# Kernel optimization log

Hardware: AMD Instinct MI355X
Metric: run time of the kernel (lower is better)

The kernel has to match this reference:

```python
import jax, jax.numpy as jnp
import numpy as np

B, XD, PD, D, H = 512, 32768, 512, 64, 128  # batch, x_dim, proj_dim, latent_dim, per_dim_hidden
G1 = 1024  # gene projector hidden (hardcoded in module)


def _init(k, shape, fan_in):
    s = 1.0 / np.sqrt(fan_in)
    return jax.random.uniform(k, shape, jnp.float32, -s, s)


def setup_inputs() -> dict:
    key = jax.random.key(0)
    ks = jax.random.split(key, 16)
    return {
        "x": jax.random.normal(ks[0], (B, XD), jnp.float32),
        "z": jax.random.normal(ks[1], (B, D), jnp.float32),
        "perm": jax.random.permutation(ks[2], B).astype(jnp.int32),
        # shared gene projector
        "Wg1": _init(ks[3], (XD, G1), XD), "bg1": _init(ks[4], (G1,), XD),
        "Wg2": _init(ks[5], (G1, PD), G1), "bg2": _init(ks[6], (PD,), G1),
        # per-dimension 3-layer MLPs, stacked over D. Layer-1 weight [PD+1, H]
        # is split into the h-part Wh and the z-part Wz (last input column).
        "Wh": _init(ks[7], (D, PD, H), PD + 1),
        "Wz": _init(ks[8], (D, H), PD + 1),
        "b1": _init(ks[9], (D, H), PD + 1),
        "W2": _init(ks[10], (D, H, H), H), "b2": _init(ks[11], (D, H), H),
        "W3": _init(ks[12], (D, H), H), "b3": _init(ks[13], (D,), H),
    }


def reference(x, z, perm, Wg1, bg1, Wg2, bg2, Wh, Wz, b1, W2, b2, W3, b3):
    elu = jax.nn.elu
    # shared gene projector (eval mode: dropout = identity, no noise)
    h = elu(elu(x @ Wg1 + bg1) @ Wg2 + bg2)            # [B, PD]
    # batched layer-1 of all D per-dim nets; h-projection computed once and
    # reused for the marginal pass via permutation (h_shuffled = h[perm]).
    hWh = jnp.einsum('bp,dph->bdh', h, Wh)             # [B, D, H]
    zWz = z[:, :, None] * Wz[None]                     # [B, D, H]

    def head(a1_pre):
        a1 = elu(a1_pre)                               # [B, D, H]
        a2 = elu(jnp.einsum('bdh,dhk->bdk', a1, W2) + b2)
        return jnp.einsum('bdh,dh->bd', a2, W3) + b3   # [B, D] scalar scores

    joint_score = head(hWh + zWz + b1)                 # T(h, z_j)
    marg_score = head(hWh[perm] + zWz + b1)            # T(h_shuffled, z_j)

    emas = jnp.ones((D,), x.dtype)                     # buffer init = ones, eval: no update
    et = jnp.mean(jnp.exp(marg_score), axis=0)         # [D]
    mi = jnp.mean(joint_score, axis=0) - jnp.log(et / emas)
    return -jnp.mean(mi)
```

## Files before the change

### kernel.cpp

```cpp
#include <hip/hip_runtime.h>
#include <hip/hip_bf16.h>
#include <math.h>

#define B_  512
#define XD_ 32768
#define PD_ 512
#define D_  64
#define H_  128
#define G1_ 1024

typedef __attribute__((ext_vector_type(8))) short short8v;
typedef __attribute__((ext_vector_type(4))) float floatx4;

__device__ __forceinline__ float eluf(float v) { return v > 0.f ? v : expm1f(v); }

__device__ __forceinline__ void split8t(const float* c, short8v& h, short8v& l) {
    unsigned hu[8], lu[8];
    #pragma unroll
    for (int j = 0; j < 8; j++) {
        unsigned u = __float_as_uint(c[j]);
        hu[j] = u & 0xFFFF0000u;
        float res = c[j] - __uint_as_float(hu[j]);
        lu[j] = __float_as_uint(res);
    }
    uint4 hp, lp;
    hp.x = __builtin_amdgcn_perm(hu[1], hu[0], 0x07060302u);
    hp.y = __builtin_amdgcn_perm(hu[3], hu[2], 0x07060302u);
    hp.z = __builtin_amdgcn_perm(hu[5], hu[4], 0x07060302u);
    hp.w = __builtin_amdgcn_perm(hu[7], hu[6], 0x07060302u);
    lp.x = __builtin_amdgcn_perm(lu[1], lu[0], 0x07060302u);
    lp.y = __builtin_amdgcn_perm(lu[3], lu[2], 0x07060302u);
    lp.z = __builtin_amdgcn_perm(lu[5], lu[4], 0x07060302u);
    lp.w = __builtin_amdgcn_perm(lu[7], lu[6], 0x07060302u);
    h = __builtin_bit_cast(short8v, hp);
    l = __builtin_bit_cast(short8v, lp);
}

__global__ __launch_bounds__(256, 2) void k_gemm1m(const float* __restrict__ x,
                                                   const float* __restrict__ Wg1,
                                                   float* __restrict__ part,
                                                   int KS) {
    __shared__ ushort Ah[4 * 128 * 8], Al[4 * 128 * 8];
    __shared__ ushort Bh[4 * 128 * 8], Bl[4 * 128 * 8];
    const int nt = blockIdx.x, mt = blockIdx.y, ks = blockIdx.z;
    const int t = threadIdx.x;
    const int w = t >> 6, lane = t & 63;
    const int q = lane >> 4, l15 = lane & 15;
    const int wr = w >> 1, wc = w & 1;
    const int kbB = t >> 6, nb = t & 63;
    const int mA = t & 127, kbA = t >> 7;
    const int k0 = ks * KS;

    const float* Ag = x + (size_t)(mt * 128 + mA) * XD_ + k0 + kbA * 8;
    const float* Bg = Wg1 + (size_t)(k0 + kbB * 8) * G1_ + nt * 128 + nb * 2;

    floatx4 acc[4][4];
    #pragma unroll
    for (int i = 0; i < 4; i++)
        #pragma unroll
        for (int j = 0; j < 4; j++) acc[i][j] = (floatx4){0.f, 0.f, 0.f, 0.f};

    float4 pa0 = *(const float4*)(Ag);
    float4 pa1 = *(const float4*)(Ag + 4);
    float4 pa2 = *(const float4*)(Ag + 16);
    float4 pa3 = *(const float4*)(Ag + 20);
    float2 pb[8];
    #pragma unroll
    for (int kk = 0; kk < 8; kk++) pb[kk] = *(const float2*)(Bg + (size_t)kk * G1_);

    for (int kt = 0; kt < KS; kt += 32) {
        float cA0[8] = {pa0.x, pa0.y, pa0.z, pa0.w, pa1.x, pa1.y, pa1.z, pa1.w};
        float cA1[8] = {pa2.x, pa2.y, pa2.z, pa2.w, pa3.x, pa3.y, pa3.z, pa3.w};
        float c0[8], c1[8];
        #pragma unroll
        for (int kk = 0; kk < 8; kk++) { c0[kk] = pb[kk].x; c1[kk] = pb[kk].y; }
        short8v ah0, al0, ah1, al1, bh0, bl0, bh1, bl1;
        split8t(cA0, ah0, al0);
        split8t(cA1, ah1, al1);
        split8t(c0, bh0, bl0);
        split8t(c1, bh1, bl1);
        if (kt + 32 < KS) {
            pa0 = *(const float4*)(Ag + kt + 32);
            pa1 = *(const float4*)(Ag + kt + 36);
            pa2 = *(const float4*)(Ag + kt + 48);
            pa3 = *(const float4*)(Ag + kt + 52);
            const float* p = Bg + (size_t)(kt + 32) * G1_;
            #pragma unroll
            for (int kk = 0; kk < 8; kk++) pb[kk] = *(const float2*)(p + (size_t)kk * G1_);
        }
        {
            int ia0 = (kbA * 128 + (mA ^ kbA)) * 8;
            int ia1 = ((kbA + 2) * 128 + (mA ^ (kbA + 2))) * 8;
            *(short8v*)&Ah[ia0] = ah0; *(short8v*)&Al[ia0] = al0;
            *(short8v*)&Ah[ia1] = ah1; *(short8v*)&Al[ia1] = al1;
            int n0i = nb * 2;
            int i0 = (kbB * 128 + (n0i ^ kbB)) * 8;
            int i1 = (kbB * 128 + ((n0i + 1) ^ kbB)) * 8;
            *(short8v*)&Bh[i0] = bh0; *(short8v*)&Bl[i0] = bl0;
            *(short8v*)&Bh[i1] = bh1; *(short8v*)&Bl[i1] = bl1;
        }
        __syncthreads();
        short8v af[4], alf[4], bf[4], blf[4];
        #pragma unroll
        for (int i = 0; i < 4; i++) {
            int m = wr * 64 + i * 16 + l15;
            int idx = (q * 128 + (m ^ q)) * 8;
            af[i]  = *(const short8v*)&Ah[idx];
            alf[i] = *(const short8v*)&Al[idx];
        }
        #pragma unroll
        for (int j = 0; j < 4; j++) {
            int n = wc * 64 + j * 16 + l15;
            int idx = (q * 128 + (n ^ q)) * 8;
            bf[j]  = *(const short8v*)&Bh[idx];
            blf[j] = *(const short8v*)&Bl[idx];
        }
        #pragma unroll
        for (int i = 0; i < 4; i++)
            #pragma unroll
            for (int j = 0; j < 4; j++) {
                acc[i][j] = __builtin_amdgcn_mfma_f32_16x16x32_bf16(af[i],  bf[j],  acc[i][j], 0, 0, 0);
                acc[i][j] = __builtin_amdgcn_mfma_f32_16x16x32_bf16(af[i],  blf[j], acc[i][j], 0, 0, 0);
                acc[i][j] = __builtin_amdgcn_mfma_f32_16x16x32_bf16(alf[i], bf[j],  acc[i][j], 0, 0, 0);
            }
        __syncthreads();
    }
    float* P = part + (size_t)ks * (B_ * G1_) + (size_t)(mt * 128) * G1_ + nt * 128;
    #pragma unroll
    for (int i = 0; i < 4; i++)
        #pragma unroll
        for (int j = 0; j < 4; j++) {
            int col = wc * 64 + j * 16 + l15;
            #pragma unroll
            for (int r = 0; r < 4; r++) {
                int row = wr * 64 + i * 16 + q * 4 + r;
                P[(size_t)row * G1_ + col] = acc[i][j][r];
            }
        }
}

__global__ __launch_bounds__(256) void k_red1(const float* __restrict__ part,
                                              const float* __restrict__ bg1,
                                              ushort* __restrict__ Gh,
                                              ushort* __restrict__ Gl,
                                              int nparts) {
    int idx = (blockIdx.x * 256 + threadIdx.x) * 8;
    const int S = B_ * G1_;
    float c[8] = {};
    for (int k = 0; k < nparts; k++) {
        const float* p = part + (size_t)k * S + idx;
        float4 v0 = *(const float4*)p, v1 = *(const float4*)(p + 4);
        c[0] += v0.x; c[1] += v0.y; c[2] += v0.z; c[3] += v0.w;
        c[4] += v1.x; c[5] += v1.y; c[6] += v1.z; c[7] += v1.w;
    }
    int cb = idx & (G1_ - 1);
    float4 b0 = *(const float4*)(bg1 + cb), b1v = *(const float4*)(bg1 + cb + 4);
    c[0] = eluf(c[0] + b0.x); c[1] = eluf(c[1] + b0.y);
    c[2] = eluf(c[2] + b0.z); c[3] = eluf(c[3] + b0.w);
    c[4] = eluf(c[4] + b1v.x); c[5] = eluf(c[5] + b1v.y);
    c[6] = eluf(c[6] + b1v.z); c[7] = eluf(c[7] + b1v.w);
    short8v h, l; split8t(c, h, l);
    *(short8v*)(Gh + idx) = h;
    *(short8v*)(Gl + idx) = l;
}

__global__ __launch_bounds__(256, 2) void k_gemm2m(const ushort* __restrict__ Gh,
                                                   const ushort* __restrict__ Gl,
                                                   const float* __restrict__ Wg2,
                                                   float* __restrict__ part2) {
    __shared__ ushort Ah[4 * 64 * 8], Al[4 * 64 * 8];
    __shared__ ushort Bh[4 * 64 * 8], Bl[4 * 64 * 8];
    const int nt = blockIdx.x, mt = blockIdx.y, ks = blockIdx.z;
    const int t = threadIdx.x;
    const int w = t >> 6, lane = t & 63;
    const int q = lane >> 4, l15 = lane & 15;
    const int kb = (t >> 4) & 3;
    const int rb = (t & 15) | (w << 4);
    const int k0 = ks * 128;

    const int cB = t & 63, g = t >> 6;

    floatx4 acc[4];
    #pragma unroll
    for (int i = 0; i < 4; i++) acc[i] = (floatx4){0.f, 0.f, 0.f, 0.f};

    for (int kt = 0; kt < 128; kt += 32) {
        {
            const ushort* pH = Gh + (size_t)(mt * 64 + rb) * G1_ + k0 + kt + kb * 8;
            const ushort* pL = Gl + (size_t)(mt * 64 + rb) * G1_ + k0 + kt + kb * 8;
            uint4 vh = *(const uint4*)pH;
            uint4 vl = *(const uint4*)pL;
            int idx = (kb * 64 + (rb ^ kb)) * 8;
            *(uint4*)&Ah[idx] = vh;
            *(uint4*)&Al[idx] = vl;
        }
        {
            float c[8];
            const float* p = Wg2 + (size_t)(k0 + kt + g * 8) * PD_ + nt * 64 + cB;
            #pragma unroll
            for (int kk = 0; kk < 8; kk++) c[kk] = p[(size_t)kk * PD_];
            short8v h, l; split8t(c, h, l);
            int idx = (g * 64 + (cB ^ g)) * 8;
            *(short8v*)&Bh[idx] = h;
            *(short8v*)&Bl[idx] = l;
        }
        __syncthreads();
        short8v af[4], alf[4], bf, blf;
        #pragma unroll
        for (int i = 0; i < 4; i++) {
            int m = i * 16 + l15;
            int idx = (q * 64 + (m ^ q)) * 8;
            af[i]  = *(const short8v*)&Ah[idx];
            alf[i] = *(const short8v*)&Al[idx];
        }
        {
            int n = w * 16 + l15;
            int idx = (q * 64 + (n ^ q)) * 8;
            bf  = *(const short8v*)&Bh[idx];
            blf = *(const short8v*)&Bl[idx];
        }
        #pragma unroll
        for (int i = 0; i < 4; i++) {
            acc[i] = __builtin_amdgcn_mfma_f32_16x16x32_bf16(af[i],  bf,  acc[i], 0, 0, 0);
            acc[i] = __builtin_amdgcn_mfma_f32_16x16x32_bf16(af[i],  blf, acc[i], 0, 0, 0);
            acc[i] = __builtin_amdgcn_mfma_f32_16x16x32_bf16(alf[i], bf,  acc[i], 0, 0, 0);
        }
        __syncthreads();
    }
    float* P = part2 + (size_t)ks * (B_ * PD_) + (size_t)(mt * 64) * PD_ + nt * 64;
    #pragma unroll
    for (int i = 0; i < 4; i++) {
        int col = w * 16 + l15;
        #pragma unroll
        for (int r = 0; r < 4; r++) {
            int row = i * 16 + q * 4 + r;
            P[(size_t)row * PD_ + col] = acc[i][r];
        }
    }
}

__global__ __launch_bounds__(256) void k_red2(const float* __restrict__ part2,
                                              const float* __restrict__ bg2,
                                              ushort* __restrict__ hh,
                                              ushort* __restrict__ hl) {
    int idx = (blockIdx.x * 256 + threadIdx.x) * 8;
    const int S = B_ * PD_;
    float c[8] = {};
    #pragma unroll
    for (int k = 0; k < 8; k++) {
        const float* p = part2 + (size_t)k * S + idx;
        float4 v0 = *(const float4*)p, v1 = *(const float4*)(p + 4);
        c[0] += v0.x; c[1] += v0.y; c[2] += v0.z; c[3] += v0.w;
        c[4] += v1.x; c[5] += v1.y; c[6] += v1.z; c[7] += v1.w;
    }
    int cb = idx & (PD_ - 1);
    float4 b0 = *(const float4*)(bg2 + cb), b1v = *(const float4*)(bg2 + cb + 4);
    c[0] = eluf(c[0] + b0.x); c[1] = eluf(c[1] + b0.y);
    c[2] = eluf(c[2] + b0.z); c[3] = eluf(c[3] + b0.w);
    c[4] = eluf(c[4] + b1v.x); c[5] = eluf(c[5] + b1v.y);
    c[6] = eluf(c[6] + b1v.z); c[7] = eluf(c[7] + b1v.w);
    short8v h, l; split8t(c, h, l);
    *(short8v*)(hh + idx) = h;
    *(short8v*)(hl + idx) = l;
}

__global__ __launch_bounds__(256, 2) void k_hwh_m(const ushort* __restrict__ hh,
                                                  const ushort* __restrict__ hl,
                                                  const float* __restrict__ Wh,
                                                  float* __restrict__ hWh) {
    __shared__ ushort Ah[4 * 64 * 8], Al[4 * 64 * 8];
    __shared__ ushort Bh[4 * 128 * 8], Bl[4 * 128 * 8];
    const int d = blockIdx.x, mt = blockIdx.y;
    const int t = threadIdx.x;
    const int w = t >> 6, lane = t & 63;
    const int q = lane >> 4, l15 = lane & 15;
    const int kb = (t >> 4) & 3;
    const int rb = (t & 15) | (w << 4);

    const ushort* AgH = hh + (size_t)(mt * 64 + rb) * PD_ + kb * 8;
    const ushort* AgL = hl + (size_t)(mt * 64 + rb) * PD_ + kb * 8;
    const float* Bg = Wh + (size_t)d * (PD_ * H_) + (size_t)(kb * 8) * H_ + rb * 2;

    floatx4 acc[4][2];
    #pragma unroll
    for (int i = 0; i < 4; i++)
        #pragma unroll
        for (int j = 0; j < 2; j++) acc[i][j] = (floatx4){0.f, 0.f, 0.f, 0.f};

    uint4 pah = *(const uint4*)(AgH);
    uint4 pal = *(const uint4*)(AgL);
    float2 pb[8];
    #pragma unroll
    for (int kk = 0; kk < 8; kk++) pb[kk] = *(const float2*)(Bg + (size_t)kk * H_);

    for (int kt = 0; kt < PD_; kt += 32) {
        float c0[8], c1[8];
        #pragma unroll
        for (int kk = 0; kk < 8; kk++) { c0[kk] = pb[kk].x; c1[kk] = pb[kk].y; }
        short8v bh0, bl0, bh1, bl1;
        split8t(c0, bh0, bl0);
        split8t(c1, bh1, bl1);
        uint4 ah = pah, al = pal;
        if (kt + 32 < PD_) {
            pah = *(const uint4*)(AgH + kt + 32);
            pal = *(const uint4*)(AgL + kt + 32);
            const float* p = Bg + (size_t)(kt + 32) * H_;
            #pragma unroll
            for (int kk = 0; kk < 8; kk++) pb[kk] = *(const float2*)(p + (size_t)kk * H_);
        }
        {
            int idx = (kb * 64 + (rb ^ kb)) * 8;
            *(uint4*)&Ah[idx] = ah;
            *(uint4*)&Al[idx] = al;
            int n0i = rb * 2;
            int i0 = (kb * 128 + (n0i ^ kb)) * 8;
            int i1 = (kb * 128 + ((n0i + 1) ^ kb)) * 8;
            *(short8v*)&Bh[i0] = bh0; *(short8v*)&Bl[i0] = bl0;
            *(short8v*)&Bh[i1] = bh1; *(short8v*)&Bl[i1] = bl1;
        }
        __syncthreads();
        short8v af[4], alf[4], bf[2], blf[2];
        #pragma unroll
        for (int i = 0; i < 4; i++) {
            int m = i * 16 + l15;
            int idx = (q * 64 + (m ^ q)) * 8;
            af[i]  = *(const short8v*)&Ah[idx];
            alf[i] = *(const short8v*)&Al[idx];
        }
        #pragma unroll
        for (int j = 0; j < 2; j++) {
            int n = w * 32 + j * 16 + l15;
            int idx = (q * 128 + (n ^ q)) * 8;
            bf[j]  = *(const short8v*)&Bh[idx];
            blf[j] = *(const short8v*)&Bl[idx];
        }
        #pragma unroll
        for (int i = 0; i < 4; i++)
            #pragma unroll
            for (int j = 0; j < 2; j++) {
                acc[i][j] = __builtin_amdgcn_mfma_f32_16x16x32_bf16(af[i],  bf[j],  acc[i][j], 0, 0, 0);
                acc[i][j] = __builtin_amdgcn_mfma_f32_16x16x32_bf16(af[i],  blf[j], acc[i][j], 0, 0, 0);
                acc[i][j] = __builtin_amdgcn_mfma_f32_16x16x32_bf16(alf[i], bf[j],  acc[i][j], 0, 0, 0);
            }
        __syncthreads();
    }
    #pragma unroll
    for (int i = 0; i < 4; i++)
        #pragma unroll
        for (int j = 0; j < 2; j++) {
            int col = w * 32 + j * 16 + l15;
            #pragma unroll
            for (int r = 0; r < 4; r++) {
                int row = i * 16 + q * 4 + r;
                int b = mt * 64 + row;
                hWh[(size_t)b * (D_ * H_) + d * H_ + col] = acc[i][j][r];
            }
        }
}

__global__ __launch_bounds__(256, 2) void k_heads(const float* __restrict__ hWh,
                                                  const float* __restrict__ z,
                                                  const int* __restrict__ perm,
                                                  const float* __restrict__ Wz,
                                                  const float* __restrict__ b1,
                                                  const float* __restrict__ W2,
                                                  const float* __restrict__ b2,
                                                  const float* __restrict__ W3,
                                                  const float* __restrict__ b3,
                                                  float* __restrict__ jpart,
                                                  float* __restrict__ epart) {
    const int chunk = blockIdx.x;
    const int d = blockIdx.y;
    const int t = threadIdx.x;
    const int b0 = chunk * 64;
    __shared__ ushort A1h[16 * 64 * 8];
    __shared__ ushort A1l[16 * 64 * 8];
    __shared__ float  BS[4096];
    ushort* Bh = (ushort*)BS;
    ushort* Bl = Bh + 4096;
    float*  sred = BS;

    const int w = t >> 6, lane = t & 63;
    const int q = lane >> 4, l15 = lane & 15;
    const int kb = (t >> 4) & 3;
    const int rb = (t & 15) | (w << 4);

    const float* W2d = W2 + (size_t)d * H_ * H_;
    const float* Wzd = Wz + d * H_;
    const float* b1d = b1 + d * H_;
    const float* b2d = b2 + d * H_;
    const float* W3d = W3 + d * H_;

    float result0 = 0.f, result1 = 0.f;
    for (int pass = 0; pass < 2; pass++) {
        {
            int i = t >> 2;
            int kt = t & 3;
            int h0 = kt * 32;
            int bb = b0 + i;
            int src = (pass == 0) ? bb : perm[bb];
            float zv = z[bb * D_ + d];
            const float* hrow = hWh + (size_t)src * (D_ * H_) + d * H_;
            #pragma unroll
            for (int kq = 0; kq < 4; kq++) {
                float c[8];
                int kbase = h0 + kq * 8;
                float4 v0 = *(const float4*)(hrow + kbase);
                float4 v1 = *(const float4*)(hrow + kbase + 4);
                float4 w0 = *(const float4*)(Wzd + kbase);
                float4 w1 = *(const float4*)(Wzd + kbase + 4);
                float4 x0 = *(const float4*)(b1d + kbase);
                float4 x1 = *(const float4*)(b1d + kbase + 4);
                c[0] = eluf(v0.x + zv * w0.x + x0.x);
                c[1] = eluf(v0.y + zv * w0.y + x0.y);
                c[2] = eluf(v0.z + zv * w0.z + x0.z);
                c[3] = eluf(v0.w + zv * w0.w + x0.w);
                c[4] = eluf(v1.x + zv * w1.x + x1.x);
                c[5] = eluf(v1.y + zv * w1.y + x1.y);
                c[6] = eluf(v1.z + zv * w1.z + x1.z);
                c[7] = eluf(v1.w + zv * w1.w + x1.w);
                short8v hv, lv; split8t(c, hv, lv);
                int idx = ((kt * 4 + kq) * 64 + (i ^ kq)) * 8;
                *(short8v*)&A1h[idx] = hv;
                *(short8v*)&A1l[idx] = lv;
            }
        }
        __syncthreads();
        floatx4 acc[4][2];
        #pragma unroll
        for (int i = 0; i < 4; i++)
            #pragma unroll
            for (int j = 0; j < 2; j++) acc[i][j] = (floatx4){0.f, 0.f, 0.f, 0.f};
        for (int kt2 = 0; kt2 < 4; kt2++) {
            {
                float c0[8], c1[8];
                const float* p = W2d + (size_t)(kt2 * 32 + kb * 8) * H_ + rb * 2;
                #pragma unroll
                for (int kk = 0; kk < 8; kk++) {
                    float2 v = *(const float2*)(p + (size_t)kk * H_);
                    c0[kk] = v.x; c1[kk] = v.y;
                }
                short8v h0v, l0v, h1v, l1v;
                split8t(c0, h0v, l0v);
                split8t(c1, h1v, l1v);
                int n0i = rb * 2;
                int i0 = (kb * 128 + (n0i ^ kb)) * 8;
                int i1 = (kb * 128 + ((n0i + 1) ^ kb)) * 8;
                *(short8v*)&Bh[i0] = h0v; *(short8v*)&Bl[i0] = l0v;
                *(short8v*)&Bh[i1] = h1v; *(short8v*)&Bl[i1] = l1v;
            }
            __syncthreads();
            short8v af[4], alf[4], bf[2], blf[2];
            #pragma unroll
            for (int i = 0; i < 4; i++) {
                int m = i * 16 + l15;
                int idx = ((kt2 * 4 + q) * 64 + (m ^ q)) * 8;
                af[i]  = *(const short8v*)&A1h[idx];
                alf[i] = *(const short8v*)&A1l[idx];
            }
            #pragma unroll
            for (int j = 0; j < 2; j++) {
                int n = w * 32 + j * 16 + l15;
                int idx = (q * 128 + (n ^ q)) * 8;
                bf[j]  = *(const short8v*)&Bh[idx];
                blf[j] = *(const short8v*)&Bl[idx];
            }
            #pragma unroll
            for (int i = 0; i < 4; i++)
                #pragma unroll
                for (int j = 0; j < 2; j++) {
                    acc[i][j] = __builtin_amdgcn_mfma_f32_16x16x32_bf16(af[i],  bf[j],  acc[i][j], 0, 0, 0);
                    acc[i][j] = __builtin_amdgcn_mfma_f32_16x16x32_bf16(af[i],  blf[j], acc[i][j], 0, 0, 0);
                    acc[i][j] = __builtin_amdgcn_mfma_f32_16x16x32_bf16(alf[i], bf[j],  acc[i][j], 0, 0, 0);
                }
            __syncthreads();
        }
        #pragma unroll
        for (int i = 0; i < 4; i++) {
            #pragma unroll
            for (int r = 0; r < 4; r++) {
                int b = i * 16 + q * 4 + r;
                float s = 0.f;
                #pragma unroll
                for (int j = 0; j < 2; j++) {
                    int col = w * 32 + j * 16 + l15;
                    float a2v = eluf(acc[i][j][r] + b2d[col]);
                    s = fmaf(a2v, W3d[col], s);
                }
                sred[b * 64 + w * 16 + l15] = s;
            }
        }
        __syncthreads();
        float val = 0.f;
        if (t < 64) {
            float s = b3[d];
            const float4* row = (const float4*)&sred[t * 64];
            #pragma unroll
            for (int c = 0; c < 16; c++) {
                float4 v = row[c];
                s += v.x + v.y + v.z + v.w;
            }
            val = (pass == 0) ? s : expf(s);
            #pragma unroll
            for (int off = 32; off > 0; off >>= 1)
                val += __shfl_down(val, off, 64);
        }
        if (t == 0) { if (pass == 0) result0 = val; else result1 = val; }
        __syncthreads();
    }
    if (t == 0) {
        jpart[d * 8 + chunk] = result0;
        epart[d * 8 + chunk] = result1;
    }
}

__global__ void k_final(const float* __restrict__ jpart,
                        const float* __restrict__ epart,
                        float* __restrict__ out) {
    int t = threadIdx.x;
    float mj = 0.f, me = 0.f;
    #pragma unroll
    for (int c = 0; c < 8; c++) { mj += jpart[t * 8 + c]; me += epart[t * 8 + c]; }
    mj *= (1.f / 512.f);
    me *= (1.f / 512.f);
    float mi = mj - logf(me);
    #pragma unroll
    for (int off = 32; off > 0; off >>= 1) mi += __shfl_down(mi, off, 64);
    if (t == 0) out[0] = -mi * (1.f / 64.f);
}

extern "C" void kernel_launch(void* const* d_in, const int* in_sizes, int n_in,
                              void* d_out, int out_size, void* d_ws, size_t ws_size,
                              hipStream_t stream) {
    const float* x   = (const float*)d_in[0];
    const float* z   = (const float*)d_in[1];
    const int*  perm = (const int*)d_in[2];
    const float* Wg1 = (const float*)d_in[3];
    const float* bg1 = (const float*)d_in[4];
    const float* Wg2 = (const float*)d_in[5];
    const float* bg2 = (const float*)d_in[6];
    const float* Wh  = (const float*)d_in[7];
    const float* Wz  = (const float*)d_in[8];
    const float* b1  = (const float*)d_in[9];
    const float* W2  = (const float*)d_in[10];
    const float* b2  = (const float*)d_in[11];
    const float* W3  = (const float*)d_in[12];
    const float* b3  = (const float*)d_in[13];
    float* out = (float*)d_out;

    const size_t PART_SLICE = (size_t)B_ * G1_ * sizeof(float);
    int nks = (ws_size >= (size_t)32 * PART_SLICE + 3145728 + 4096) ? 32 : 16;
    const int KS = XD_ / nks;
    const size_t partBytes = (size_t)nks * PART_SLICE;

    char* base = (char*)d_ws;
    float* part  = (float*)base;
    float* hWh   = (float*)base;
    float* part2 = (float*)(base + 16777216);
    ushort* Gh   = (ushort*)(base + partBytes);
    ushort* Gl   = Gh + 524288;
    ushort* hh   = (ushort*)(base + partBytes + 2097152);
    ushort* hl   = hh + 262144;
    float* jpart = (float*)(base + partBytes + 3145728);
    float* epart = jpart + 512;

    k_gemm1m<<<dim3(8, 4, nks), 256, 0, stream>>>(x, Wg1, part, KS);
    k_red1<<<256, 256, 0, stream>>>(part, bg1, Gh, Gl, nks);
    k_gemm2m<<<dim3(8, 8, 8), 256, 0, stream>>>(Gh, Gl, Wg2, part2);
    k_red2<<<128, 256, 0, stream>>>(part2, bg2, hh, hl);
    k_hwh_m<<<dim3(64, 8), 256, 0, stream>>>(hh, hl, Wh, hWh);
    k_heads<<<dim3(8, 64), 256, 0, stream>>>(hWh, z, perm, Wz, b1, W2, b2, W3, b3,
                                             jpart, epart);
    k_final<<<1, 64, 0, stream>>>(jpart, epart, out);
}
```

Baseline: 421.0 us.

## Transpose x up front and double-buffer the split-bf16 first GEMM

Adds a transpose kernel that writes x as a K-major copy, so the first projector GEMM can load both operands with row-contiguous float2 accesses. The new GEMM kernel uses double-buffered LDS with register prefetch and one barrier per K step, and runs with 16 K-splits. This targets uncoalesced or strided A loads and load/compute serialization in the dominant GEMM. In exchange it adds an extra 64MB read and write pass over x, needs a larger workspace, and keeps the old path as a fallback when the workspace is too small.

```diff
diff --git a/kernel.cpp b/kernel.cpp
--- a/kernel.cpp
+++ b/kernel.cpp
@@ -34,6 +34,141 @@
     lp.w = __builtin_amdgcn_perm(lu[7], lu[6], 0x07060302u);
     h = __builtin_bit_cast(short8v, hp);
     l = __builtin_bit_cast(short8v, lp);
+}
+
+__global__ __launch_bounds__(256) void k_tr(const float* __restrict__ x,
+                                            float* __restrict__ xT) {
+    __shared__ float tile[64][65];
+    const int k0 = blockIdx.x * 64;
+    const int m0 = blockIdx.y * 64;
+    const int t = threadIdx.x;
+    const int tk = t & 63, tg = t >> 6;
+    #pragma unroll
+    for (int i = 0; i < 16; i++) {
+        int r = tg * 16 + i;
+        tile[r][tk] = x[(size_t)(m0 + r) * XD_ + k0 + tk];
+    }
+    __syncthreads();
+    #pragma unroll
+    for (int i = 0; i < 16; i++) {
+        int r = tg * 16 + i;
+        xT[(size_t)(k0 + r) * B_ + m0 + tk] = tile[tk][r];
+    }
+}
+
+__global__ __launch_bounds__(256, 2) void k_gemm1t(const float* __restrict__ xT,
+                                                   const float* __restrict__ Wg1,
+                                                   float* __restrict__ part,
+                                                   int KS) {
+    __shared__ ushort Ah[2][4 * 128 * 8], Al[2][4 * 128 * 8];
+    __shared__ ushort Bh[2][4 * 128 * 8], Bl[2][4 * 128 * 8];
+    const int nt = blockIdx.x, mt = blockIdx.y, ks = blockIdx.z;
+    const int t = threadIdx.x;
+    const int w = t >> 6, lane = t & 63;
+    const int q = lane >> 4, l15 = lane & 15;
+    const int wr = w >> 1, wc = w & 1;
+    const int kbS = t >> 6, pr = t & 63;
+    const int k0 = ks * KS;
+
+    const float* Ag = xT + (size_t)(k0 + kbS * 8) * B_ + mt * 128 + pr * 2;
+    const float* Bg = Wg1 + (size_t)(k0 + kbS * 8) * G1_ + nt * 128 + pr * 2;
+
+    floatx4 acc[4][4];
+    #pragma unroll
+    for (int i = 0; i < 4; i++)
+        #pragma unroll
+        for (int j = 0; j < 4; j++) acc[i][j] = (floatx4){0.f, 0.f, 0.f, 0.f};
+
+    float2 pa[8], pb[8];
+    #pragma unroll
+    for (int kk = 0; kk < 8; kk++) {
+        pa[kk] = *(const float2*)(Ag + (size_t)kk * B_);
+        pb[kk] = *(const float2*)(Bg + (size_t)kk * G1_);
+    }
+
+    auto stage = [&](int buf) {
+        float a0[8], a1[8], c0[8], c1[8];
+        #pragma unroll
+        for (int kk = 0; kk < 8; kk++) {
+            a0[kk] = pa[kk].x; a1[kk] = pa[kk].y;
+            c0[kk] = pb[kk].x; c1[kk] = pb[kk].y;
+        }
+        short8v ah0, al0, ah1, al1, bh0, bl0, bh1, bl1;
+        split8t(a0, ah0, al0); split8t(a1, ah1, al1);
+        split8t(c0, bh0, bl0); split8t(c1, bh1, bl1);
+        int n0 = pr * 2;
+        int ia0 = (kbS * 128 + (n0 ^ kbS)) * 8;
+        int ia1 = (kbS * 128 + ((n0 + 1) ^ kbS)) * 8;
+        *(short8v*)&Ah[buf][ia0] = ah0; *(short8v*)&Al[buf][ia0] = al0;
+        *(short8v*)&Ah[buf][ia1] = ah1; *(short8v*)&Al[buf][ia1] = al1;
+        *(short8v*)&Bh[buf][ia0] = bh0; *(short8v*)&Bl[buf][ia0] = bl0;
+        *(short8v*)&Bh[buf][ia1] = bh1; *(short8v*)&Bl[buf][ia1] = bl1;
+    };
+
+    auto mma = [&](int buf) {
+        short8v af[4], alf[4], bf[4], blf[4];
+        #pragma unroll
+        for (int i = 0; i < 4; i++) {
+            int m = wr * 64 + i * 16 + l15;
+            int idx = (q * 128 + (m ^ q)) * 8;
+            af[i]  = *(const short8v*)&Ah[buf][idx];
+            alf[i] = *(const short8v*)&Al[buf][idx];
+        }
+        #pragma unroll
+        for (int j = 0; j < 4; j++) {
+            int n = wc * 64 + j * 16 + l15;
+            int idx = (q * 128 + (n ^ q)) * 8;
+            bf[j]  = *(const short8v*)&Bh[buf][idx];
+            blf[j] = *(const short8v*)&Bl[buf][idx];
+        }
+        #pragma unroll
+        for (int i = 0; i < 4; i++)
+            #pragma unroll
+            for (int j = 0; j < 4; j++) {
+                acc[i][j] = __builtin_amdgcn_mfma_f32_16x16x32_bf16(af[i],  bf[j],  acc[i][j], 0, 0, 0);
+                acc[i][j] = __builtin_amdgcn_mfma_f32_16x16x32_bf16(af[i],  blf[j], acc[i][j], 0, 0, 0);
+                acc[i][j] = __builtin_amdgcn_mfma_f32_16x16x32_bf16(alf[i], bf[j],  acc[i][j], 0, 0, 0);
+            }
+    };
+
+    stage(0);
+    #pragma unroll
+    for (int kk = 0; kk < 8; kk++) {
+        pa[kk] = *(const float2*)(Ag + (size_t)(32 + kk) * B_);
+        pb[kk] = *(const float2*)(Bg + (size_t)(32 + kk) * G1_);
+    }
+    asm volatile("s_waitcnt lgkmcnt(0)" ::: "memory");
+    __builtin_amdgcn_s_barrier();
+
+    const int NT = KS >> 5;
+    for (int it = 0; it < NT - 1; it++) {
+        const int cur = it & 1;
+        stage(cur ^ 1);
+        if (it + 2 < NT) {
+            #pragma unroll
+            for (int kk = 0; kk < 8; kk++) {
+                pa[kk] = *(const float2*)(Ag + (size_t)((it + 2) * 32 + kk) * B_);
+                pb[kk] = *(const float2*)(Bg + (size_t)((it + 2) * 32 + kk) * G1_);
+            }
+        }
+        mma(cur);
+        asm volatile("s_waitcnt lgkmcnt(0)" ::: "memory");
+        __builtin_amdgcn_s_barrier();
+    }
+    mma((NT - 1) & 1);
+
+    float* P = part + (size_t)ks * (B_ * G1_) + (size_t)(mt * 128) * G1_ + nt * 128;
+    #pragma unroll
+    for (int i = 0; i < 4; i++)
+        #pragma unroll
+        for (int j = 0; j < 4; j++) {
+            int col = wc * 64 + j * 16 + l15;
+            #pragma unroll
+            for (int r = 0; r < 4; r++) {
+                int row = wr * 64 + i * 16 + q * 4 + r;
+                P[(size_t)row * G1_ + col] = acc[i][j][r];
+            }
+        }
 }
 
 __global__ __launch_bounds__(256, 2) void k_gemm1m(const float* __restrict__ x,
@@ -548,28 +683,54 @@
     const float* b3  = (const float*)d_in[13];
     float* out = (float*)d_out;
 
+    char* base = (char*)d_ws;
     const size_t PART_SLICE = (size_t)B_ * G1_ * sizeof(float);
-    int nks = (ws_size >= (size_t)32 * PART_SLICE + 3145728 + 4096) ? 32 : 16;
-    const int KS = XD_ / nks;
-    const size_t partBytes = (size_t)nks * PART_SLICE;
-
-    char* base = (char*)d_ws;
-    float* part  = (float*)base;
-    float* hWh   = (float*)base;
-    float* part2 = (float*)(base + 16777216);
-    ushort* Gh   = (ushort*)(base + partBytes);
-    ushort* Gl   = Gh + 524288;
-    ushort* hh   = (ushort*)(base + partBytes + 2097152);
-    ushort* hl   = hh + 262144;
-    float* jpart = (float*)(base + partBytes + 3145728);
-    float* epart = jpart + 512;
-
-    k_gemm1m<<<dim3(8, 4, nks), 256, 0, stream>>>(x, Wg1, part, KS);
-    k_red1<<<256, 256, 0, stream>>>(part, bg1, Gh, Gl, nks);
-    k_gemm2m<<<dim3(8, 8, 8), 256, 0, stream>>>(Gh, Gl, Wg2, part2);
-    k_red2<<<128, 256, 0, stream>>>(part2, bg2, hh, hl);
-    k_hwh_m<<<dim3(64, 8), 256, 0, stream>>>(hh, hl, Wh, hWh);
-    k_heads<<<dim3(8, 64), 256, 0, stream>>>(hWh, z, perm, Wz, b1, W2, b2, W3, b3,
-                                             jpart, epart);
-    k_final<<<1, 64, 0, stream>>>(jpart, epart, out);
-}
+
+    const size_t NEW_NEED = 16 * PART_SLICE + 67108864ull + 2097152 + 1048576 + 4096;
+
+    if (ws_size >= NEW_NEED) {
+        float* part  = (float*)base;
+        float* xT    = (float*)(base + 33554432);
+        float* hWh   = (float*)base;
+        float* part2 = (float*)(base + 16777216);
+        ushort* Gh   = (ushort*)(base + 100663296);
+        ushort* Gl   = Gh + 524288;
+        ushort* hh   = (ushort*)(base + 102760448);
+        ushort* hl   = hh + 262144;
+        float* jpart = (float*)(base + 103809024);
+        float* epart = jpart + 512;
+
+        k_tr<<<dim3(512, 8), 256, 0, stream>>>(x, xT);
+        k_gemm1t<<<dim3(8, 4, 16), 256, 0, stream>>>(xT, Wg1, part, XD_ / 16);
+        k_red1<<<256, 256, 0, stream>>>(part, bg1, Gh, Gl, 16);
+        k_gemm2m<<<dim3(8, 8, 8), 256, 0, stream>>>(Gh, Gl, Wg2, part2);
+        k_red2<<<128, 256, 0, stream>>>(part2, bg2, hh, hl);
+        k_hwh_m<<<dim3(64, 8), 256, 0, stream>>>(hh, hl, Wh, hWh);
+        k_heads<<<dim3(8, 64), 256, 0, stream>>>(hWh, z, perm, Wz, b1, W2, b2, W3, b3,
+                                                 jpart, epart);
+        k_final<<<1, 64, 0, stream>>>(jpart, epart, out);
+    } else {
+        int nks = (ws_size >= (size_t)32 * PART_SLICE + 3145728 + 4096) ? 32 : 16;
+        const int KS = XD_ / nks;
+        const size_t partBytes = (size_t)nks * PART_SLICE;
+
+        float* part  = (float*)base;
+        float* hWh   = (float*)base;
+        float* part2 = (float*)(base + 16777216);
+        ushort* Gh   = (ushort*)(base + partBytes);
+        ushort* Gl   = Gh + 524288;
+        ushort* hh   = (ushort*)(base + partBytes + 2097152);
+        ushort* hl   = hh + 262144;
+        float* jpart = (float*)(base + partBytes + 3145728);
+        float* epart = jpart + 512;
+
+        k_gemm1m<<<dim3(8, 4, nks), 256, 0, stream>>>(x, Wg1, part, KS);
+        k_red1<<<256, 256, 0, stream>>>(part, bg1, Gh, Gl, nks);
+        k_gemm2m<<<dim3(8, 8, 8), 256, 0, stream>>>(Gh, Gl, Wg2, part2);
+        k_red2<<<128, 256, 0, stream>>>(part2, bg2, hh, hl);
+        k_hwh_m<<<dim3(64, 8), 256, 0, stream>>>(hh, hl, Wh, hWh);
+        k_heads<<<dim3(8, 64), 256, 0, stream>>>(hWh, z, perm, Wz, b1, W2, b2, W3, b3,
+                                                 jpart, epart);
+        k_final<<<1, 64, 0, stream>>>(jpart, epart, out);
+    }
+}
```

After: 432.9 us. +2.8%, slower.
